# Performance work log

Hardware: AMD Instinct MI355X
Metric: run time of the kernel (lower is better)

## Reference

```python
import jax, jax.numpy as jnp
import numpy as np

CHANNELS = 128
M_MODES = 64
B = 128
N = 4096


def setup_inputs() -> dict:
    key = jax.random.key(0)
    k1, k2, k3 = jax.random.split(key, 3)
    h = jax.random.normal(k1, (B * N, CHANNELS), dtype=jnp.float32)
    U = jax.random.normal(k2, (B, N, M_MODES), dtype=jnp.float32)
    W = jax.random.normal(k3, (M_MODES, CHANNELS, CHANNELS), dtype=jnp.float32) * 0.02
    ptr = jnp.arange(B + 1, dtype=jnp.int64) * N  # equal-size segments
    return {"h": h, "U": U, "W": W, "ptr": ptr}


def reference(h, U, W, ptr):
    # U: [B, N, m]; h: [B*N, C]; W: [m, C, C]
    b, n, m = U.shape
    hb = h.reshape(b, n, -1)                              # [B, N, C]
    h_hat = jnp.einsum('bnm,bnc->bmc', U, hb)             # U^T h per graph
    out_hat = jnp.einsum('bmc,mco->bmo', h_hat, W)        # per-mode channel mix
    out = jnp.einsum('bnm,bmo->bno', U, out_hat)          # back to node space
    return out.reshape(h.shape)
```

## Files before the change

### kernel.cpp

```cpp
#include <hip/hip_runtime.h>

#define CH 128
#define MM 64
#define BB 128
#define NN 4096
#define KSPLIT 4
#define KCHUNK (NN / KSPLIT)
#define KSTEP 32
#define NSTEP (KCHUNK / KSTEP)

#define UBUF (KSTEP * MM)
#define HBUF (KSTEP * CH)
#define BUF  (UBUF + HBUF)

typedef __bf16 bf16x8 __attribute__((ext_vector_type(8)));
typedef float  f32x4  __attribute__((ext_vector_type(4)));

#define AS1(p) ((const __attribute__((address_space(1))) void*)(p))
#define AS3(p) ((__attribute__((address_space(3))) void*)(p))

__device__ __forceinline__ void gl_lds16(const float* g, float* l) {
    __builtin_amdgcn_global_load_lds(AS1(g), AS3(l), 16, 0, 0);
}

__global__ __launch_bounds__(256, 2) void k1_uth(const float* __restrict__ U,
                                                 const float* __restrict__ h,
                                                 float* __restrict__ hhp) {
    __shared__ float lds[3 * BUF];

    const int tid  = threadIdx.x;
    const int lane = tid & 63;
    const int wv   = tid >> 6;
    const int b    = blockIdx.x >> 2;
    const int ks   = blockIdx.x & 3;
    const int k0   = ks * KCHUNK;

    const int l15 = lane & 15;
    const int g   = lane >> 4;
    const int lk  = g * 8;

    const float* Ub = U + ((size_t)b * NN + k0) * MM;
    const float* hb = h + ((size_t)b * NN + k0) * CH;

    auto stage = [&](int s, int t) {
        float* dst = &lds[s * BUF];
        const float* us = Ub + (size_t)t * KSTEP * MM;
        const float* hs = hb + (size_t)t * KSTEP * CH;
        gl_lds16(us + tid * 4,        dst + tid * 4);
        gl_lds16(us + 1024 + tid * 4, dst + 1024 + tid * 4);
        gl_lds16(hs + tid * 4,        dst + UBUF + tid * 4);
        gl_lds16(hs + 1024 + tid * 4, dst + UBUF + 1024 + tid * 4);
        gl_lds16(hs + 2048 + tid * 4, dst + UBUF + 2048 + tid * 4);
        gl_lds16(hs + 3072 + tid * 4, dst + UBUF + 3072 + tid * 4);
    };

    f32x4 acc[4][2];
    #pragma unroll
    for (int t = 0; t < 4; ++t)
        #pragma unroll
        for (int ci = 0; ci < 2; ++ci)
            acc[t][ci] = (f32x4){0.f, 0.f, 0.f, 0.f};

    auto compute = [&](int s) {
        const float* P  = &lds[s * BUF];
        const float* Pa = P + lk * 64 + 2 * l15;
        const float* Pb = P + UBUF + lk * 128 + wv * 32 + 2 * l15;
        bf16x8 af[4], bfr[2];
        #pragma unroll
        for (int j = 0; j < 8; ++j) {
            float2 a0 = *(const float2*)(Pa + j * 64);
            float2 a1 = *(const float2*)(Pa + j * 64 + 32);
            float2 bv = *(const float2*)(Pb + j * 128);
            af[0][j]  = (__bf16)a0.x;
            af[1][j]  = (__bf16)a0.y;
            af[2][j]  = (__bf16)a1.x;
            af[3][j]  = (__bf16)a1.y;
            bfr[0][j] = (__bf16)bv.x;
            bfr[1][j] = (__bf16)bv.y;
        }
        #pragma unroll
        for (int t = 0; t < 4; ++t)
            #pragma unroll
            for (int ci = 0; ci < 2; ++ci)
                acc[t][ci] = __builtin_amdgcn_mfma_f32_16x16x32_bf16(
                    af[t], bfr[ci], acc[t][ci], 0, 0, 0);
    };

    stage(0, 0);
    stage(1, 1);
    #pragma unroll 1
    for (int t = 0; t < NSTEP; ++t) {
        if (t + 2 < NSTEP) {
            stage((t + 2) % 3, t + 2);
            asm volatile("s_waitcnt vmcnt(12)" ::: "memory");
        } else if (t + 1 < NSTEP) {
            asm volatile("s_waitcnt vmcnt(6)" ::: "memory");
        } else {
            asm volatile("s_waitcnt vmcnt(0)" ::: "memory");
        }
        __builtin_amdgcn_s_barrier();
        __builtin_amdgcn_sched_barrier(0);
        compute(t % 3);
        __builtin_amdgcn_s_barrier();
    }

    float* dst = hhp + (size_t)(b * KSPLIT + ks) * MM * CH + wv * 32 + 2 * l15;
    #pragma unroll
    for (int t = 0; t < 4; ++t)
        #pragma unroll
        for (int r = 0; r < 4; ++r) {
            const int m = (t >> 1) * 32 + 2 * (g * 4 + r) + (t & 1);
            *(float2*)(dst + (size_t)m * CH) =
                make_float2(acc[t][0][r], acc[t][1][r]);
        }
}

__global__ __launch_bounds__(256) void k2_mix(const float* __restrict__ hhp,
                                              const float* __restrict__ W,
                                              __bf16* __restrict__ ohf) {
    __shared__ float hs[16][CH];
    const int tid  = threadIdx.x;
    const int o    = tid & 127;
    const int half = tid >> 7;
    const int m    = blockIdx.x;
    const int b0   = blockIdx.y * 16;

    #pragma unroll
    for (int i = 0; i < 8; ++i) {
        const int b = b0 + half * 8 + i;
        const float* src = hhp + ((size_t)(b * KSPLIT) * MM + m) * CH + o;
        float s = 0.f;
        #pragma unroll
        for (int ksi = 0; ksi < KSPLIT; ++ksi)
            s += src[(size_t)ksi * MM * CH];
        hs[half * 8 + i][o] = s;
    }
    __syncthreads();

    float acc[8];
    #pragma unroll
    for (int i = 0; i < 8; ++i) acc[i] = 0.f;

    const float* Wm = W + (size_t)m * CH * CH;
    for (int c = 0; c < CH; ++c) {
        const float w = Wm[c * CH + o];
        #pragma unroll
        for (int i = 0; i < 8; ++i) acc[i] += hs[half * 8 + i][c] * w;
    }

    const int mt      = m >> 5;
    const int m5      = m & 31;
    const int lane_hi = m5 >> 3;
    const int j       = m5 & 7;
    const int ot      = o >> 4;
    const int lane    = lane_hi * 16 + (o & 15);
    const size_t eidx = ((size_t)(mt * 8 + ot) * 64 + lane) * 8 + j;

    #pragma unroll
    for (int i = 0; i < 8; ++i) {
        const int b = b0 + half * 8 + i;
        ohf[(size_t)b * 8192 + eidx] = (__bf16)acc[i];
    }
}

__global__ __launch_bounds__(256) void k3_back(const float* __restrict__ U,
                                               const __bf16* __restrict__ ohf,
                                               float* __restrict__ out) {
    const int tid  = threadIdx.x;
    const int lane = tid & 63;
    const int wv   = tid >> 6;
    const int n0   = blockIdx.x * 64;
    const int b    = blockIdx.y;

    const bf16x8* ohfb = (const bf16x8*)(ohf + (size_t)b * 8192);
    bf16x8 bf[2][8];
    #pragma unroll
    for (int mt = 0; mt < 2; ++mt)
        #pragma unroll
        for (int ot = 0; ot < 8; ++ot)
            bf[mt][ot] = ohfb[(mt * 8 + ot) * 64 + lane];

    const float* arow = U + ((size_t)b * NN + n0 + wv * 16 + (lane & 15)) * MM
                          + ((lane >> 4) << 3);
    bf16x8 af[2];
    #pragma unroll
    for (int mt = 0; mt < 2; ++mt) {
        float4 a0 = *(const float4*)(arow + mt * 32);
        float4 a1 = *(const float4*)(arow + mt * 32 + 4);
        af[mt][0] = (__bf16)a0.x; af[mt][1] = (__bf16)a0.y;
        af[mt][2] = (__bf16)a0.z; af[mt][3] = (__bf16)a0.w;
        af[mt][4] = (__bf16)a1.x; af[mt][5] = (__bf16)a1.y;
        af[mt][6] = (__bf16)a1.z; af[mt][7] = (__bf16)a1.w;
    }

    f32x4 acc[8];
    #pragma unroll
    for (int ot = 0; ot < 8; ++ot) acc[ot] = (f32x4){0.f, 0.f, 0.f, 0.f};

    #pragma unroll
    for (int ot = 0; ot < 8; ++ot) {
        acc[ot] = __builtin_amdgcn_mfma_f32_16x16x32_bf16(af[0], bf[0][ot], acc[ot], 0, 0, 0);
        acc[ot] = __builtin_amdgcn_mfma_f32_16x16x32_bf16(af[1], bf[1][ot], acc[ot], 0, 0, 0);
    }

    float* dst = out + ((size_t)b * NN + n0 + wv * 16 + (lane >> 4) * 4) * CH + (lane & 15);
    #pragma unroll
    for (int ot = 0; ot < 8; ++ot)
        #pragma unroll
        for (int r = 0; r < 4; ++r)
            dst[(size_t)r * CH + ot * 16] = acc[ot][r];
}

extern "C" void kernel_launch(void* const* d_in, const int* in_sizes, int n_in,
                              void* d_out, int out_size, void* d_ws, size_t ws_size,
                              hipStream_t stream) {
    const float* h = (const float*)d_in[0];
    const float* U = (const float*)d_in[1];
    const float* W = (const float*)d_in[2];
    float* out = (float*)d_out;

    float*  hhp = (float*)d_out;
    __bf16* ohf = (__bf16*)d_ws;

    k1_uth<<<BB * KSPLIT, 256, 0, stream>>>(U, h, hhp);
    k2_mix<<<dim3(MM, BB / 16), 256, 0, stream>>>(hhp, W, ohf);
    k3_back<<<dim3(NN / 64, BB), 256, 0, stream>>>(U, ohf, out);
}
```

Baseline: 212.4 us.

## Fuse three kernels into one with per-graph inter-block spin barriers

Merges the U^T h reduction, the per-mode channel mix and the back-projection into a single kernel launched with 512 threads per block and four blocks per graph. The blocks of a graph synchronize through atomic counters in workspace, which is reset by a memset before launch. Each block then reduces its share of modes from the partial sums, mixes them with W, and projects back its own quarter of the nodes. This removes two launches and their inter-kernel gaps, and spreads the mixing step across more blocks. It relies on all four blocks of a group being co-resident, otherwise the spin-wait can deadlock, and it adds a memset plus spin-wait overhead.

```diff
diff --git a/kernel.cpp b/kernel.cpp
--- a/kernel.cpp
+++ b/kernel.cpp
@@ -4,14 +4,13 @@
 #define MM 64
 #define BB 128
 #define NN 4096
-#define KSPLIT 4
-#define KCHUNK (NN / KSPLIT)
+#define QN 1024
 #define KSTEP 32
-#define NSTEP (KCHUNK / KSTEP)
-
+#define NSTEP (QN / KSTEP)
 #define UBUF (KSTEP * MM)
 #define HBUF (KSTEP * CH)
 #define BUF  (UBUF + HBUF)
+#define MMCH (MM * CH)
 
 typedef __bf16 bf16x8 __attribute__((ext_vector_type(8)));
 typedef float  f32x4  __attribute__((ext_vector_type(4)));
@@ -23,21 +22,38 @@
     __builtin_amdgcn_global_load_lds(AS1(g), AS3(l), 16, 0, 0);
 }
 
-__global__ __launch_bounds__(256, 2) void k1_uth(const float* __restrict__ U,
-                                                 const float* __restrict__ h,
-                                                 float* __restrict__ hhp) {
+__device__ __forceinline__ void group_sync(int* c, int tid) {
+    __threadfence();
+    __syncthreads();
+    if (tid == 0) {
+        atomicAdd(c, 1);
+        while (atomicAdd(c, 0) < 4) __builtin_amdgcn_s_sleep(2);
+    }
+    __syncthreads();
+    __threadfence();
+}
+
+__global__ __launch_bounds__(512, 2) void fused_gsc(const float* __restrict__ U,
+                                                    const float* __restrict__ h,
+                                                    const float* __restrict__ W,
+                                                    float* __restrict__ part,
+                                                    __bf16* __restrict__ ohf,
+                                                    int* __restrict__ cnt,
+                                                    float* __restrict__ out) {
     __shared__ float lds[3 * BUF];
 
     const int tid  = threadIdx.x;
     const int lane = tid & 63;
     const int wv   = tid >> 6;
     const int b    = blockIdx.x >> 2;
-    const int ks   = blockIdx.x & 3;
-    const int k0   = ks * KCHUNK;
-
-    const int l15 = lane & 15;
-    const int g   = lane >> 4;
-    const int lk  = g * 8;
+    const int q    = blockIdx.x & 3;
+    const int k0   = q * QN;
+
+    const int l15  = lane & 15;
+    const int g    = lane >> 4;
+    const int lk   = g * 8;
+    const int half = wv >> 2;
+    const int cq   = wv & 3;
 
     const float* Ub = U + ((size_t)b * NN + k0) * MM;
     const float* hb = h + ((size_t)b * NN + k0) * CH;
@@ -47,43 +63,37 @@
         const float* us = Ub + (size_t)t * KSTEP * MM;
         const float* hs = hb + (size_t)t * KSTEP * CH;
         gl_lds16(us + tid * 4,        dst + tid * 4);
-        gl_lds16(us + 1024 + tid * 4, dst + 1024 + tid * 4);
         gl_lds16(hs + tid * 4,        dst + UBUF + tid * 4);
-        gl_lds16(hs + 1024 + tid * 4, dst + UBUF + 1024 + tid * 4);
         gl_lds16(hs + 2048 + tid * 4, dst + UBUF + 2048 + tid * 4);
-        gl_lds16(hs + 3072 + tid * 4, dst + UBUF + 3072 + tid * 4);
     };
 
-    f32x4 acc[4][2];
+    f32x4 acc1[2][2];
     #pragma unroll
-    for (int t = 0; t < 4; ++t)
+    for (int p = 0; p < 2; ++p)
         #pragma unroll
         for (int ci = 0; ci < 2; ++ci)
-            acc[t][ci] = (f32x4){0.f, 0.f, 0.f, 0.f};
-
-    auto compute = [&](int s) {
+            acc1[p][ci] = (f32x4){0.f, 0.f, 0.f, 0.f};
+
+    auto compute1 = [&](int s) {
         const float* P  = &lds[s * BUF];
-        const float* Pa = P + lk * 64 + 2 * l15;
-        const float* Pb = P + UBUF + lk * 128 + wv * 32 + 2 * l15;
-        bf16x8 af[4], bfr[2];
+        const float* Pa = P + lk * 64 + half * 32 + 2 * l15;
+        const float* Pb = P + UBUF + lk * 128 + cq * 32 + 2 * l15;
+        bf16x8 af[2], bfr[2];
         #pragma unroll
         for (int j = 0; j < 8; ++j) {
-            float2 a0 = *(const float2*)(Pa + j * 64);
-            float2 a1 = *(const float2*)(Pa + j * 64 + 32);
+            float2 av = *(const float2*)(Pa + j * 64);
             float2 bv = *(const float2*)(Pb + j * 128);
-            af[0][j]  = (__bf16)a0.x;
-            af[1][j]  = (__bf16)a0.y;
-            af[2][j]  = (__bf16)a1.x;
-            af[3][j]  = (__bf16)a1.y;
+            af[0][j]  = (__bf16)av.x;
+            af[1][j]  = (__bf16)av.y;
             bfr[0][j] = (__bf16)bv.x;
             bfr[1][j] = (__bf16)bv.y;
         }
         #pragma unroll
-        for (int t = 0; t < 4; ++t)
+        for (int p = 0; p < 2; ++p)
             #pragma unroll
             for (int ci = 0; ci < 2; ++ci)
-                acc[t][ci] = __builtin_amdgcn_mfma_f32_16x16x32_bf16(
-                    af[t], bfr[ci], acc[t][ci], 0, 0, 0);
+                acc1[p][ci] = __builtin_amdgcn_mfma_f32_16x16x32_bf16(
+                    af[p], bfr[ci], acc1[p][ci], 0, 0, 0);
     };
 
     stage(0, 0);
@@ -92,123 +102,103 @@
     for (int t = 0; t < NSTEP; ++t) {
         if (t + 2 < NSTEP) {
             stage((t + 2) % 3, t + 2);
-            asm volatile("s_waitcnt vmcnt(12)" ::: "memory");
+            asm volatile("s_waitcnt vmcnt(6)" ::: "memory");
         } else if (t + 1 < NSTEP) {
-            asm volatile("s_waitcnt vmcnt(6)" ::: "memory");
+            asm volatile("s_waitcnt vmcnt(3)" ::: "memory");
         } else {
             asm volatile("s_waitcnt vmcnt(0)" ::: "memory");
         }
         __builtin_amdgcn_s_barrier();
         __builtin_amdgcn_sched_barrier(0);
-        compute(t % 3);
+        compute1(t % 3);
         __builtin_amdgcn_s_barrier();
     }
 
-    float* dst = hhp + (size_t)(b * KSPLIT + ks) * MM * CH + wv * 32 + 2 * l15;
+    {
+        float* pdst = part + (size_t)(b * 4 + q) * MMCH + cq * 32 + 2 * l15;
+        #pragma unroll
+        for (int p = 0; p < 2; ++p)
+            #pragma unroll
+            for (int r = 0; r < 4; ++r) {
+                const int m = half * 32 + 2 * (g * 4 + r) + p;
+                *(float2*)(pdst + (size_t)m * CH) =
+                    make_float2(acc1[p][0][r], acc1[p][1][r]);
+            }
+    }
+
+    group_sync(&cnt[b * 2 + 0], tid);
+
+    {
+        const int lm = tid >> 5;
+        const int c4 = (tid & 31) * 4;
+        const float* p0 = part + (size_t)(b * 4) * MMCH
+                               + (size_t)(q * 16 + lm) * CH + c4;
+        float4 s0 = *(const float4*)(p0);
+        float4 s1 = *(const float4*)(p0 + MMCH);
+        float4 s2 = *(const float4*)(p0 + 2 * MMCH);
+        float4 s3 = *(const float4*)(p0 + 3 * MMCH);
+        float4 sm = make_float4(s0.x + s1.x + s2.x + s3.x,
+                                s0.y + s1.y + s2.y + s3.y,
+                                s0.z + s1.z + s2.z + s3.z,
+                                s0.w + s1.w + s2.w + s3.w);
+        *(float4*)&lds[lm * CH + c4] = sm;
+    }
+    __syncthreads();
+
     #pragma unroll
-    for (int t = 0; t < 4; ++t)
-        #pragma unroll
-        for (int r = 0; r < 4; ++r) {
-            const int m = (t >> 1) * 32 + 2 * (g * 4 + r) + (t & 1);
-            *(float2*)(dst + (size_t)m * CH) =
-                make_float2(acc[t][0][r], acc[t][1][r]);
-        }
-}
-
-__global__ __launch_bounds__(256) void k2_mix(const float* __restrict__ hhp,
-                                              const float* __restrict__ W,
-                                              __bf16* __restrict__ ohf) {
-    __shared__ float hs[16][CH];
-    const int tid  = threadIdx.x;
-    const int o    = tid & 127;
-    const int half = tid >> 7;
-    const int m    = blockIdx.x;
-    const int b0   = blockIdx.y * 16;
-
-    #pragma unroll
-    for (int i = 0; i < 8; ++i) {
-        const int b = b0 + half * 8 + i;
-        const float* src = hhp + ((size_t)(b * KSPLIT) * MM + m) * CH + o;
-        float s = 0.f;
-        #pragma unroll
-        for (int ksi = 0; ksi < KSPLIT; ++ksi)
-            s += src[(size_t)ksi * MM * CH];
-        hs[half * 8 + i][o] = s;
-    }
-    __syncthreads();
-
-    float acc[8];
-    #pragma unroll
-    for (int i = 0; i < 8; ++i) acc[i] = 0.f;
-
-    const float* Wm = W + (size_t)m * CH * CH;
-    for (int c = 0; c < CH; ++c) {
-        const float w = Wm[c * CH + o];
-        #pragma unroll
-        for (int i = 0; i < 8; ++i) acc[i] += hs[half * 8 + i][c] * w;
-    }
-
-    const int mt      = m >> 5;
-    const int m5      = m & 31;
-    const int lane_hi = m5 >> 3;
-    const int j       = m5 & 7;
-    const int ot      = o >> 4;
-    const int lane    = lane_hi * 16 + (o & 15);
-    const size_t eidx = ((size_t)(mt * 8 + ot) * 64 + lane) * 8 + j;
-
-    #pragma unroll
-    for (int i = 0; i < 8; ++i) {
-        const int b = b0 + half * 8 + i;
-        ohf[(size_t)b * 8192 + eidx] = (__bf16)acc[i];
-    }
-}
-
-__global__ __launch_bounds__(256) void k3_back(const float* __restrict__ U,
-                                               const __bf16* __restrict__ ohf,
-                                               float* __restrict__ out) {
-    const int tid  = threadIdx.x;
-    const int lane = tid & 63;
-    const int wv   = tid >> 6;
-    const int n0   = blockIdx.x * 64;
-    const int b    = blockIdx.y;
-
-    const bf16x8* ohfb = (const bf16x8*)(ohf + (size_t)b * 8192);
-    bf16x8 bf[2][8];
-    #pragma unroll
-    for (int mt = 0; mt < 2; ++mt)
+    for (int s = 0; s < 2; ++s) {
+        const int lm = wv * 2 + s;
+        const int m  = q * 16 + lm;
+        const float* Wm = W + (size_t)m * CH * CH;
+        float a0 = 0.f, a1 = 0.f;
+        #pragma unroll 4
+        for (int c = 0; c < CH; ++c) {
+            const float hhv = lds[lm * CH + c];
+            a0 += hhv * Wm[c * CH + lane];
+            a1 += hhv * Wm[c * CH + 64 + lane];
+        }
+        const int mt  = m >> 5;
+        const int lhi = (m & 31) >> 3;
+        const int j   = m & 7;
+        const int fl  = lhi * 16 + l15;
+        ohf[(size_t)b * 8192 + ((size_t)(mt * 8 + g)     * 64 + fl) * 8 + j] = (__bf16)a0;
+        ohf[(size_t)b * 8192 + ((size_t)(mt * 8 + 4 + g) * 64 + fl) * 8 + j] = (__bf16)a1;
+    }
+
+    group_sync(&cnt[b * 2 + 1], tid);
+
+    const __bf16* ohfb = ohf + (size_t)b * 8192;
+    #pragma unroll 1
+    for (int it = 0; it < 8; ++it) {
+        const int n0 = q * QN + it * 128 + wv * 16;
+        const float* arow = U + ((size_t)b * NN + n0 + l15) * MM + (g << 3);
+        bf16x8 af2[2];
+        #pragma unroll
+        for (int mt = 0; mt < 2; ++mt) {
+            float4 a0 = *(const float4*)(arow + mt * 32);
+            float4 a1 = *(const float4*)(arow + mt * 32 + 4);
+            af2[mt][0] = (__bf16)a0.x; af2[mt][1] = (__bf16)a0.y;
+            af2[mt][2] = (__bf16)a0.z; af2[mt][3] = (__bf16)a0.w;
+            af2[mt][4] = (__bf16)a1.x; af2[mt][5] = (__bf16)a1.y;
+            af2[mt][6] = (__bf16)a1.z; af2[mt][7] = (__bf16)a1.w;
+        }
+        f32x4 acc3[8];
+        #pragma unroll
+        for (int ot = 0; ot < 8; ++ot) acc3[ot] = (f32x4){0.f, 0.f, 0.f, 0.f};
+        #pragma unroll
+        for (int ot = 0; ot < 8; ++ot) {
+            bf16x8 b0 = *(const bf16x8*)(ohfb + ((size_t)(0 * 8 + ot) * 64 + lane) * 8);
+            bf16x8 b1 = *(const bf16x8*)(ohfb + ((size_t)(1 * 8 + ot) * 64 + lane) * 8);
+            acc3[ot] = __builtin_amdgcn_mfma_f32_16x16x32_bf16(af2[0], b0, acc3[ot], 0, 0, 0);
+            acc3[ot] = __builtin_amdgcn_mfma_f32_16x16x32_bf16(af2[1], b1, acc3[ot], 0, 0, 0);
+        }
+        float* dst = out + ((size_t)b * NN + n0 + g * 4) * CH + l15;
         #pragma unroll
         for (int ot = 0; ot < 8; ++ot)
-            bf[mt][ot] = ohfb[(mt * 8 + ot) * 64 + lane];
-
-    const float* arow = U + ((size_t)b * NN + n0 + wv * 16 + (lane & 15)) * MM
-                          + ((lane >> 4) << 3);
-    bf16x8 af[2];
-    #pragma unroll
-    for (int mt = 0; mt < 2; ++mt) {
-        float4 a0 = *(const float4*)(arow + mt * 32);
-        float4 a1 = *(const float4*)(arow + mt * 32 + 4);
-        af[mt][0] = (__bf16)a0.x; af[mt][1] = (__bf16)a0.y;
-        af[mt][2] = (__bf16)a0.z; af[mt][3] = (__bf16)a0.w;
-        af[mt][4] = (__bf16)a1.x; af[mt][5] = (__bf16)a1.y;
-        af[mt][6] = (__bf16)a1.z; af[mt][7] = (__bf16)a1.w;
-    }
-
-    f32x4 acc[8];
-    #pragma unroll
-    for (int ot = 0; ot < 8; ++ot) acc[ot] = (f32x4){0.f, 0.f, 0.f, 0.f};
-
-    #pragma unroll
-    for (int ot = 0; ot < 8; ++ot) {
-        acc[ot] = __builtin_amdgcn_mfma_f32_16x16x32_bf16(af[0], bf[0][ot], acc[ot], 0, 0, 0);
-        acc[ot] = __builtin_amdgcn_mfma_f32_16x16x32_bf16(af[1], bf[1][ot], acc[ot], 0, 0, 0);
-    }
-
-    float* dst = out + ((size_t)b * NN + n0 + wv * 16 + (lane >> 4) * 4) * CH + (lane & 15);
-    #pragma unroll
-    for (int ot = 0; ot < 8; ++ot)
-        #pragma unroll
-        for (int r = 0; r < 4; ++r)
-            dst[(size_t)r * CH + ot * 16] = acc[ot][r];
+            #pragma unroll
+            for (int r = 0; r < 4; ++r)
+                dst[(size_t)r * CH + ot * 16] = acc3[ot][r];
+    }
 }
 
 extern "C" void kernel_launch(void* const* d_in, const int* in_sizes, int n_in,
@@ -219,10 +209,10 @@
     const float* W = (const float*)d_in[2];
     float* out = (float*)d_out;
 
-    float*  hhp = (float*)d_out;
-    __bf16* ohf = (__bf16*)d_ws;
-
-    k1_uth<<<BB * KSPLIT, 256, 0, stream>>>(U, h, hhp);
-    k2_mix<<<dim3(MM, BB / 16), 256, 0, stream>>>(hhp, W, ohf);
-    k3_back<<<dim3(NN / 64, BB), 256, 0, stream>>>(U, ohf, out);
-}
+    float*  part = (float*)d_ws;
+    __bf16* ohf  = (__bf16*)(part + (size_t)BB * 4 * MMCH);
+    int*    cnt  = (int*)(ohf + (size_t)BB * 8192);
+
+    hipMemsetAsync(cnt, 0, BB * 2 * sizeof(int), stream);
+    fused_gsc<<<BB * 4, 512, 0, stream>>>(U, h, W, part, ohf, cnt, out);
+}
```

New measurement: 708.7 us. +233.6%, slower.
